# Kernel tuning notes

Hardware: AMD Instinct MI355X
Metric: run time of the kernel (lower is better)

Reference implementation:

```python
import jax, jax.numpy as jnp
import numpy as np

N_NODES = 100000
N_EDGES = 10000
N_PAIRS = 1600000
F = 128


def setup_inputs() -> dict:
    key = jax.random.key(0)
    ks = jax.random.split(key, 7)
    x = jax.random.normal(ks[0], (N_NODES, F), dtype=jnp.float32)
    action = jax.random.uniform(ks[1], (N_NODES, 3), dtype=jnp.float32)
    W_msg = jax.random.normal(ks[2], (F, F), dtype=jnp.float32) * (1.0 / np.sqrt(F))
    W_upd = jax.random.normal(ks[3], (F, F), dtype=jnp.float32) * (1.0 / np.sqrt(F))
    b_upd = jax.random.normal(ks[4], (F,), dtype=jnp.float32) * 0.02
    pair_node = jax.random.randint(ks[5], (N_PAIRS,), 0, N_NODES, dtype=jnp.int32)
    pair_edge = jax.random.randint(ks[6], (N_PAIRS,), 0, N_EDGES, dtype=jnp.int32)
    return {"x": x, "action": action, "W_msg": W_msg, "W_upd": W_upd,
            "b_upd": b_upd, "pair_node": pair_node, "pair_edge": pair_edge}


def _v2v_mean(m, pair_node, pair_edge):
    # v2e: mean of incident node features per hyperedge, then
    # e2v: mean of incident hyperedge features per node.
    ones = jnp.ones((pair_node.shape[0],), dtype=m.dtype)
    edge_deg = jax.ops.segment_sum(ones, pair_edge, num_segments=N_EDGES)
    node_deg = jax.ops.segment_sum(ones, pair_node, num_segments=N_NODES)
    # gather node features to incidence pairs, reduce into edges  [E, F]
    e_feat = jax.ops.segment_sum(m[pair_node], pair_edge, num_segments=N_EDGES)
    e_feat = e_feat / jnp.maximum(edge_deg, 1.0)[:, None]
    # gather edge features back to pairs, reduce into nodes       [N, F]
    v_feat = jax.ops.segment_sum(e_feat[pair_edge], pair_node, num_segments=N_NODES)
    v_feat = v_feat / jnp.maximum(node_deg, 1.0)[:, None]
    return v_feat


def reference(x, action, W_msg, W_upd, b_upd, pair_node, pair_edge):
    send = action[:, 0] + action[:, 2]      # [N]
    receive = action[:, 0] + action[:, 1]   # [N]
    m_ji = x @ W_msg.T                       # lin_message (no bias)
    m_ji = jax.nn.gelu(m_ji, approximate=False)  # dropout=0 (eval)
    m_ji = m_ji * send[:, None]
    m_i = _v2v_mean(m_ji, pair_node, pair_edge)
    m_i = m_i * receive[:, None]
    h_i = jax.nn.gelu(x @ W_upd.T + b_upd + m_i, approximate=False)
    return h_i
```

## Files before the change

### kernel.cpp

```cpp
#include <hip/hip_runtime.h>

#define N_NODESC 100000
#define N_EDGESC 10000
#define N_PAIRSC 1600000
#define FDIM 128

#define NB 200
#define EPB 50
#define NPB 500
#define ECAP2 8704
#define PA_CHUNK 8192
#define PA_NCH ((N_PAIRSC + PA_CHUNK - 1) / PA_CHUNK)
#define MSG_BLKS 782

typedef short bf16x8 __attribute__((ext_vector_type(8)));
typedef float f32x4 __attribute__((ext_vector_type(4)));
typedef float f32x2 __attribute__((ext_vector_type(2)));
typedef int i32x4 __attribute__((ext_vector_type(4)));
typedef unsigned u32x4 __attribute__((ext_vector_type(4)));

__device__ __forceinline__ unsigned short f2b(float f) {
  unsigned u = __float_as_uint(f);
  u += 0x7fffu + ((u >> 16) & 1u);
  return (unsigned short)(u >> 16);
}
__device__ __forceinline__ float b2f(unsigned short b) {
  return __uint_as_float(((unsigned)b) << 16);
}
__device__ __forceinline__ unsigned pack2(float a, float b) {
  return (unsigned)f2b(a) | ((unsigned)f2b(b) << 16);
}
__device__ __forceinline__ float gelu_fast(float z) {
  float z2 = z * z;
  float w = fmaf(0.044715f, z2, 1.0f);
  float e = __expf(1.5957691216f * z * w);
  return z * e * __builtin_amdgcn_rcpf(e + 1.0f);
}
__device__ __forceinline__ bf16x8 ldA(const float* p) {
  float4 u0 = *(const float4*)p;
  float4 u1 = *(const float4*)(p + 4);
  u32x4 w = {pack2(u0.x, u0.y), pack2(u0.z, u0.w), pack2(u1.x, u1.y), pack2(u1.z, u1.w)};
  return __builtin_bit_cast(bf16x8, w);
}

__global__ __launch_bounds__(256) void k_prep(const float* __restrict__ action,
                                              const float* __restrict__ wmsg, const float* __restrict__ wupd,
                                              short* __restrict__ wmsgb, short* __restrict__ wupdb,
                                              float* __restrict__ send, float* __restrict__ recv,
                                              int* __restrict__ gcure, int* __restrict__ gcurn) {
  int i = blockIdx.x * 256 + threadIdx.x;
  if (i < FDIM * FDIM) {
    wmsgb[i] = (short)f2b(wmsg[i]);
    wupdb[i] = (short)f2b(wupd[i]);
  }
  if (i < N_NODESC) {
    float a0 = action[i * 3 + 0], a1 = action[i * 3 + 1], a2 = action[i * 3 + 2];
    send[i] = a0 + a2;
    recv[i] = a0 + a1;
  }
  if (i < NB) {
    gcure[i] = i * ECAP2;
    gcurn[i] = i * ECAP2;
  }
}

__device__ __forceinline__ int wave_incl_scan(int v, int lane) {
#pragma unroll
  for (int d = 1; d < 64; d <<= 1) {
    int n = __shfl_up(v, d, 64);
    if (lane >= d) v += n;
  }
  return v;
}

__global__ __launch_bounds__(256) void k_part_msg(const int* __restrict__ pn, const int* __restrict__ pe,
                                                  int* __restrict__ gcure, int* __restrict__ gcurn,
                                                  unsigned* __restrict__ buckE, unsigned* __restrict__ buckN,
                                                  const float* __restrict__ x, const short* __restrict__ wb,
                                                  const float* __restrict__ send,
                                                  unsigned char* __restrict__ mji8) {
  __shared__ unsigned stage[PA_CHUNK];
  __shared__ int ce[NB], cn[NB];
  int t = threadIdx.x;
  if (blockIdx.x < PA_NCH) {
    for (int i = t; i < NB; i += 256) { ce[i] = 0; cn[i] = 0; }
    __syncthreads();
    long long base = (long long)blockIdx.x * PA_CHUNK;
    int nItems = (int)(((long long)N_PAIRSC - base) < PA_CHUNK ? (N_PAIRSC - base) : PA_CHUNK);
    for (int q = t; q < PA_CHUNK / 4; q += 256) {
      long long idx = base + (long long)q * 4;
      if (idx >= N_PAIRSC) break;
      i32x4 e4 = __builtin_nontemporal_load((const i32x4*)(pe + idx));
      i32x4 v4 = __builtin_nontemporal_load((const i32x4*)(pn + idx));
#pragma unroll
      for (int j = 0; j < 4; j++) {
        unsigned ee = (unsigned)e4[j], vv = (unsigned)v4[j];
        stage[q + j * (PA_CHUNK / 4)] = (ee << 17) | vv;
        atomicAdd(&ce[ee / EPB], 1);
        atomicAdd(&cn[vv / NPB], 1);
      }
    }
    __syncthreads();
    for (int i = t; i < NB; i += 256) {
      ce[i] = atomicAdd(&gcure[i], ce[i]);
      cn[i] = atomicAdd(&gcurn[i], cn[i]);
    }
    __syncthreads();
    for (int i = t; i < PA_CHUNK; i += 256) {
      int q = i & (PA_CHUNK / 4 - 1), j = i >> 11;
      long long idx = base + (long long)q * 4 + j;
      if (idx >= N_PAIRSC) continue;
      unsigned u = stage[i];
      unsigned ee = u >> 17, vv = u & 0x1FFFF;
      int p1 = atomicAdd(&ce[ee / EPB], 1);
      buckE[p1] = u;
      int p2 = atomicAdd(&cn[vv / NPB], 1);
      buckN[p2] = (vv << 14) | ee;
    }
    (void)nItems;
  } else {
    int gw = ((int)(blockIdx.x - PA_NCH) * 256 + t) >> 6;
    int lane = t & 63;
    if (gw >= N_NODESC / 32) return;
    int rb = gw * 32;
    int lr = lane & 15, lg = lane >> 4;

    bf16x8 A0[4], A1[4];
    const float* xrow0 = x + (size_t)(rb + lr) * FDIM + lg * 8;
    const float* xrow1 = xrow0 + 16 * FDIM;
#pragma unroll
    for (int kk = 0; kk < 4; kk++) {
      A0[kk] = ldA(xrow0 + kk * 32);
      A1[kk] = ldA(xrow1 + kk * 32);
    }
    float sv0[4], sv1[4];
#pragma unroll
    for (int j = 0; j < 4; j++) {
      sv0[j] = send[rb + lg * 4 + j];
      sv1[j] = send[rb + 16 + lg * 4 + j];
    }
#pragma unroll
    for (int c = 0; c < 8; c++) {
      f32x4 acc0 = {0.f, 0.f, 0.f, 0.f}, acc1 = {0.f, 0.f, 0.f, 0.f};
      const short* wrow = wb + (size_t)(16 * c + lr) * FDIM + lg * 8;
#pragma unroll
      for (int kk = 0; kk < 4; kk++) {
        bf16x8 B = *(const bf16x8*)(wrow + kk * 32);
        acc0 = __builtin_amdgcn_mfma_f32_16x16x32_bf16(A0[kk], B, acc0, 0, 0, 0);
        acc1 = __builtin_amdgcn_mfma_f32_16x16x32_bf16(A1[kk], B, acc1, 0, 0, 0);
      }
      int col = 16 * c + lr;
#pragma unroll
      for (int j = 0; j < 4; j++) {
        float m0 = gelu_fast(acc0[j]) * sv0[j];
        float m1 = gelu_fast(acc1[j]) * sv1[j];
        int row0 = rb + lg * 4 + j;
        mji8[(size_t)row0 * FDIM + col] =
            (unsigned char)(__builtin_amdgcn_cvt_pk_fp8_f32(m0, m0, 0, false) & 0xFF);
        mji8[(size_t)(row0 + 16) * FDIM + col] =
            (unsigned char)(__builtin_amdgcn_cvt_pk_fp8_f32(m1, m1, 0, false) & 0xFF);
      }
    }
  }
}

__global__ __launch_bounds__(256) void k_fine_e(const unsigned* __restrict__ buckE,
                                                const int* __restrict__ gcure,
                                                int* __restrict__ ecnt, int* __restrict__ eoff,
                                                int* __restrict__ sn) {
  __shared__ int cnt_s[EPB], cur_s[EPB];
  int b = blockIdx.x, t = threadIdx.x;
  int lo = b * EPB, beg = b * ECAP2, end = gcure[b];
  if (t < EPB) cnt_s[t] = 0;
  __syncthreads();
  for (int i = beg + t; i < end; i += 256)
    atomicAdd(&cnt_s[(int)(buckE[i] >> 17) - lo], 1);
  __syncthreads();
  if (t < 64) {
    int v = (t < EPB) ? cnt_s[t] : 0;
    int inc = wave_incl_scan(v, t);
    if (t < EPB) cur_s[t] = beg + inc - v;
  }
  __syncthreads();
  if (t < EPB) {
    ecnt[lo + t] = cnt_s[t];
    eoff[lo + t] = cur_s[t];
  }
  __syncthreads();
  for (int i = beg + t; i < end; i += 256) {
    unsigned u = buckE[i];
    int key = (int)(u >> 17) - lo;
    int pos = atomicAdd(&cur_s[key], 1);
    sn[pos] = (int)(u & 0x1FFFF);
  }
}

__global__ __launch_bounds__(256) void k_edge_fineN(const unsigned* __restrict__ buckN,
                                                    const int* __restrict__ gcurn,
                                                    int* __restrict__ ncnt, int* __restrict__ noff,
                                                    int* __restrict__ se,
                                                    const unsigned char* __restrict__ mji8,
                                                    const int* __restrict__ sn,
                                                    const int* __restrict__ eoff, const int* __restrict__ ecnt,
                                                    unsigned char* __restrict__ efeat8) {
  __shared__ int cnt_s[NPB], cur_s[NPB];
  int t = threadIdx.x;
  if (blockIdx.x < NB) {
    int b = blockIdx.x;
    int lo = b * NPB, beg = b * ECAP2, end = gcurn[b];
    for (int i = t; i < NPB; i += 256) cnt_s[i] = 0;
    __syncthreads();
    for (int i = beg + t; i < end; i += 256)
      atomicAdd(&cnt_s[(int)(buckN[i] >> 14) - lo], 1);
    __syncthreads();
    if (t < 64) {
      int carry = beg;
#pragma unroll
      for (int base = 0; base < NPB; base += 64) {
        int idx = base + t;
        int v = (idx < NPB) ? cnt_s[idx] : 0;
        int inc = wave_incl_scan(v, t);
        if (idx < NPB) cur_s[idx] = carry + inc - v;
        carry += __shfl(inc, 63, 64);
      }
    }
    __syncthreads();
    for (int i = t; i < NPB; i += 256) {
      ncnt[lo + i] = cnt_s[i];
      noff[lo + i] = cur_s[i];
    }
    __syncthreads();
    for (int i = beg + t; i < end; i += 256) {
      unsigned u = buckN[i];
      int key = (int)(u >> 14) - lo;
      int pos = atomicAdd(&cur_s[key], 1);
      se[pos] = (int)(u & 0x3FFF);
    }
  } else {
    int wave = (int)(blockIdx.x - NB) * 4 + (t >> 6);
    int lane = t & 63;
    int half = lane >> 5, sub2 = (lane >> 4) & 1, c4 = lane & 15;
    int edge = wave * 2 + half;
    if (edge >= N_EDGESC) return;
    int beg = eoff[edge], cnt = ecnt[edge];
    f32x2 a0 = {0.f, 0.f}, a1 = {0.f, 0.f}, a2 = {0.f, 0.f}, a3 = {0.f, 0.f};
#pragma unroll 4
    for (int p = sub2; p < cnt; p += 2) {
      int node = sn[beg + p];
      uint2 u = ((const uint2*)(mji8 + (size_t)node * FDIM))[c4];
      a0 += __builtin_amdgcn_cvt_pk_f32_fp8(u.x, false);
      a1 += __builtin_amdgcn_cvt_pk_f32_fp8(u.x, true);
      a2 += __builtin_amdgcn_cvt_pk_f32_fp8(u.y, false);
      a3 += __builtin_amdgcn_cvt_pk_f32_fp8(u.y, true);
    }
    a0[0] += __shfl_xor(a0[0], 16, 64); a0[1] += __shfl_xor(a0[1], 16, 64);
    a1[0] += __shfl_xor(a1[0], 16, 64); a1[1] += __shfl_xor(a1[1], 16, 64);
    a2[0] += __shfl_xor(a2[0], 16, 64); a2[1] += __shfl_xor(a2[1], 16, 64);
    a3[0] += __shfl_xor(a3[0], 16, 64); a3[1] += __shfl_xor(a3[1], 16, 64);
    if (sub2 == 0) {
      float inv = 1.0f / fmaxf((float)cnt, 1.0f);
      uint2 o;
      o.x = (unsigned)__builtin_amdgcn_cvt_pk_fp8_f32(a0[0] * inv, a0[1] * inv, 0, false);
      o.x = (unsigned)__builtin_amdgcn_cvt_pk_fp8_f32(a1[0] * inv, a1[1] * inv, (int)o.x, true);
      o.y = (unsigned)__builtin_amdgcn_cvt_pk_fp8_f32(a2[0] * inv, a2[1] * inv, 0, false);
      o.y = (unsigned)__builtin_amdgcn_cvt_pk_fp8_f32(a3[0] * inv, a3[1] * inv, (int)o.y, true);
      ((uint2*)(efeat8 + (size_t)edge * FDIM))[c4] = o;
    }
  }
}

__global__ __launch_bounds__(256) void k_node(const unsigned char* __restrict__ efeat8, const int* __restrict__ se,
                                              const int* __restrict__ noff, const int* __restrict__ ncnt,
                                              const float* __restrict__ recv, short* __restrict__ mi) {
  int wave = blockIdx.x * 4 + (threadIdx.x >> 6);
  int lane = threadIdx.x & 63;
  int sub = lane >> 4, c4 = lane & 15;
  int node = wave * 4 + sub;
  int beg = noff[node], cnt = ncnt[node];
  f32x2 a0 = {0.f, 0.f}, a1 = {0.f, 0.f}, a2 = {0.f, 0.f}, a3 = {0.f, 0.f};
#pragma unroll 4
  for (int p = 0; p < cnt; p++) {
    int e = se[beg + p];
    uint2 u = ((const uint2*)(efeat8 + (size_t)e * FDIM))[c4];
    a0 += __builtin_amdgcn_cvt_pk_f32_fp8(u.x, false);
    a1 += __builtin_amdgcn_cvt_pk_f32_fp8(u.x, true);
    a2 += __builtin_amdgcn_cvt_pk_f32_fp8(u.y, false);
    a3 += __builtin_amdgcn_cvt_pk_f32_fp8(u.y, true);
  }
  float s = recv[node] / fmaxf((float)cnt, 1.0f);
  u32x4 o;
  o[0] = pack2(a0[0] * s, a0[1] * s);
  o[1] = pack2(a1[0] * s, a1[1] * s);
  o[2] = pack2(a2[0] * s, a2[1] * s);
  o[3] = pack2(a3[0] * s, a3[1] * s);
  ((u32x4*)(mi + (size_t)node * FDIM))[c4] = o;
}

__global__ __launch_bounds__(256) void k_gemm_upd(const float* __restrict__ x, const short* __restrict__ wb,
                                                  const float* __restrict__ bias, const short* __restrict__ mi,
                                                  float* __restrict__ out) {
  int gw = (blockIdx.x * 256 + threadIdx.x) >> 6;
  int lane = threadIdx.x & 63;
  if (gw >= N_NODESC / 32) return;
  int rb = gw * 32;
  int lr = lane & 15, lg = lane >> 4;

  bf16x8 A0[4], A1[4];
  const float* xrow0 = x + (size_t)(rb + lr) * FDIM + lg * 8;
  const float* xrow1 = xrow0 + 16 * FDIM;
#pragma unroll
  for (int kk = 0; kk < 4; kk++) {
    A0[kk] = ldA(xrow0 + kk * 32);
    A1[kk] = ldA(xrow1 + kk * 32);
  }

#pragma unroll
  for (int c = 0; c < 8; c++) {
    f32x4 acc0 = {0.f, 0.f, 0.f, 0.f}, acc1 = {0.f, 0.f, 0.f, 0.f};
    const short* wrow = wb + (size_t)(16 * c + lr) * FDIM + lg * 8;
#pragma unroll
    for (int kk = 0; kk < 4; kk++) {
      bf16x8 B = *(const bf16x8*)(wrow + kk * 32);
      acc0 = __builtin_amdgcn_mfma_f32_16x16x32_bf16(A0[kk], B, acc0, 0, 0, 0);
      acc1 = __builtin_amdgcn_mfma_f32_16x16x32_bf16(A1[kk], B, acc1, 0, 0, 0);
    }
    int col = 16 * c + lr;
    float bc = bias[col];
#pragma unroll
    for (int j = 0; j < 4; j++) {
      int row0 = rb + lg * 4 + j;
      float z0 = acc0[j] + bc + b2f(((const unsigned short*)mi)[(size_t)row0 * FDIM + col]);
      float z1 = acc1[j] + bc + b2f(((const unsigned short*)mi)[(size_t)(row0 + 16) * FDIM + col]);
      __builtin_nontemporal_store(gelu_fast(z0), &out[(size_t)row0 * FDIM + col]);
      __builtin_nontemporal_store(gelu_fast(z1), &out[(size_t)(row0 + 16) * FDIM + col]);
    }
  }
}

extern "C" void kernel_launch(void* const* d_in, const int* in_sizes, int n_in,
                              void* d_out, int out_size, void* d_ws, size_t ws_size,
                              hipStream_t stream) {
  const float* x = (const float*)d_in[0];
  const float* action = (const float*)d_in[1];
  const float* wmsg = (const float*)d_in[2];
  const float* wupd = (const float*)d_in[3];
  const float* bupd = (const float*)d_in[4];
  const int* pn = (const int*)d_in[5];
  const int* pe = (const int*)d_in[6];
  float* out = (float*)d_out;

  char* p = (char*)d_ws;
  auto alloc = [&](size_t bytes) -> char* {
    char* r = p;
    p += (bytes + 255) & ~(size_t)255;
    return r;
  };
  unsigned char* mji8 = (unsigned char*)alloc((size_t)N_NODESC * FDIM);
  short* mi = (short*)alloc((size_t)N_NODESC * FDIM * 2);
  unsigned char* efeat8 = (unsigned char*)alloc((size_t)N_EDGESC * FDIM);
  int* sn = (int*)alloc((size_t)NB * ECAP2 * 4);
  int* se = (int*)alloc((size_t)NB * ECAP2 * 4);
  short* wmsgb = (short*)alloc(FDIM * FDIM * 2);
  short* wupdb = (short*)alloc(FDIM * FDIM * 2);
  float* send = (float*)alloc(N_NODESC * 4);
  float* recv = (float*)alloc(N_NODESC * 4);
  int* ecnt = (int*)alloc(N_EDGESC * 4);
  int* eoff = (int*)alloc(N_EDGESC * 4);
  int* ncnt = (int*)alloc(N_NODESC * 4);
  int* noff = (int*)alloc(N_NODESC * 4);
  int* gcure = (int*)alloc(NB * 4);
  int* gcurn = (int*)alloc(NB * 4);

  unsigned* buckE = (unsigned*)mi;
  unsigned* buckN = buckE + (size_t)NB * ECAP2;

  k_prep<<<391, 256, 0, stream>>>(action, wmsg, wupd, wmsgb, wupdb, send, recv, gcure, gcurn);
  k_part_msg<<<PA_NCH + MSG_BLKS, 256, 0, stream>>>(pn, pe, gcure, gcurn, buckE, buckN,
                                                    x, wmsgb, send, mji8);
  k_fine_e<<<NB, 256, 0, stream>>>(buckE, gcure, ecnt, eoff, sn);
  k_edge_fineN<<<NB + 1250, 256, 0, stream>>>(buckN, gcurn, ncnt, noff, se,
                                              mji8, sn, eoff, ecnt, efeat8);
  k_node<<<6250, 256, 0, stream>>>(efeat8, se, noff, ncnt, recv, mi);
  k_gemm_upd<<<782, 256, 0, stream>>>(x, wupdb, bupd, mi, out);
}
```

Measured before the change: 164.4 us.

## Store node messages as fp8, shrink partition chunks, use per-wave LDS bucket counters

```diff
diff --git a/kernel.cpp b/kernel.cpp
--- a/kernel.cpp
+++ b/kernel.cpp
@@ -9,7 +9,7 @@
 #define EPB 50
 #define NPB 500
 #define ECAP2 8704
-#define PA_CHUNK 8192
+#define PA_CHUNK 4096
 #define PA_NCH ((N_PAIRSC + PA_CHUNK - 1) / PA_CHUNK)
 #define MSG_BLKS 782
 
@@ -80,13 +80,13 @@
                                                   const float* __restrict__ send,
                                                   unsigned char* __restrict__ mji8) {
   __shared__ unsigned stage[PA_CHUNK];
-  __shared__ int ce[NB], cn[NB];
+  __shared__ int ce4[4][NB], cn4[4][NB];
   int t = threadIdx.x;
   if (blockIdx.x < PA_NCH) {
-    for (int i = t; i < NB; i += 256) { ce[i] = 0; cn[i] = 0; }
+    int w = t >> 6;
+    for (int i = t; i < 4 * NB; i += 256) { ((int*)ce4)[i] = 0; ((int*)cn4)[i] = 0; }
     __syncthreads();
     long long base = (long long)blockIdx.x * PA_CHUNK;
-    int nItems = (int)(((long long)N_PAIRSC - base) < PA_CHUNK ? (N_PAIRSC - base) : PA_CHUNK);
     for (int q = t; q < PA_CHUNK / 4; q += 256) {
       long long idx = base + (long long)q * 4;
       if (idx >= N_PAIRSC) break;
@@ -96,28 +96,31 @@
       for (int j = 0; j < 4; j++) {
         unsigned ee = (unsigned)e4[j], vv = (unsigned)v4[j];
         stage[q + j * (PA_CHUNK / 4)] = (ee << 17) | vv;
-        atomicAdd(&ce[ee / EPB], 1);
-        atomicAdd(&cn[vv / NPB], 1);
+        atomicAdd(&ce4[w][ee / EPB], 1);
+        atomicAdd(&cn4[w][vv / NPB], 1);
       }
     }
     __syncthreads();
-    for (int i = t; i < NB; i += 256) {
-      ce[i] = atomicAdd(&gcure[i], ce[i]);
-      cn[i] = atomicAdd(&gcurn[i], cn[i]);
+    if (t < NB) {
+      int c0 = ce4[0][t], c1 = ce4[1][t], c2 = ce4[2][t], c3 = ce4[3][t];
+      int b0 = atomicAdd(&gcure[t], c0 + c1 + c2 + c3);
+      ce4[0][t] = b0; ce4[1][t] = b0 + c0; ce4[2][t] = b0 + c0 + c1; ce4[3][t] = b0 + c0 + c1 + c2;
+      int d0 = cn4[0][t], d1 = cn4[1][t], d2 = cn4[2][t], d3 = cn4[3][t];
+      int b1 = atomicAdd(&gcurn[t], d0 + d1 + d2 + d3);
+      cn4[0][t] = b1; cn4[1][t] = b1 + d0; cn4[2][t] = b1 + d0 + d1; cn4[3][t] = b1 + d0 + d1 + d2;
     }
     __syncthreads();
     for (int i = t; i < PA_CHUNK; i += 256) {
-      int q = i & (PA_CHUNK / 4 - 1), j = i >> 11;
+      int q = i & (PA_CHUNK / 4 - 1), j = i >> 10;
       long long idx = base + (long long)q * 4 + j;
       if (idx >= N_PAIRSC) continue;
       unsigned u = stage[i];
       unsigned ee = u >> 17, vv = u & 0x1FFFF;
-      int p1 = atomicAdd(&ce[ee / EPB], 1);
+      int p1 = atomicAdd(&ce4[w][ee / EPB], 1);
       buckE[p1] = u;
-      int p2 = atomicAdd(&cn[vv / NPB], 1);
+      int p2 = atomicAdd(&cn4[w][vv / NPB], 1);
       buckN[p2] = (vv << 14) | ee;
     }
-    (void)nItems;
   } else {
     int gw = ((int)(blockIdx.x - PA_NCH) * 256 + t) >> 6;
     int lane = t & 63;
@@ -271,7 +274,7 @@
 
 __global__ __launch_bounds__(256) void k_node(const unsigned char* __restrict__ efeat8, const int* __restrict__ se,
                                               const int* __restrict__ noff, const int* __restrict__ ncnt,
-                                              const float* __restrict__ recv, short* __restrict__ mi) {
+                                              const float* __restrict__ recv, unsigned char* __restrict__ mi8) {
   int wave = blockIdx.x * 4 + (threadIdx.x >> 6);
   int lane = threadIdx.x & 63;
   int sub = lane >> 4, c4 = lane & 15;
@@ -288,16 +291,17 @@
     a3 += __builtin_amdgcn_cvt_pk_f32_fp8(u.y, true);
   }
   float s = recv[node] / fmaxf((float)cnt, 1.0f);
-  u32x4 o;
-  o[0] = pack2(a0[0] * s, a0[1] * s);
-  o[1] = pack2(a1[0] * s, a1[1] * s);
-  o[2] = pack2(a2[0] * s, a2[1] * s);
-  o[3] = pack2(a3[0] * s, a3[1] * s);
-  ((u32x4*)(mi + (size_t)node * FDIM))[c4] = o;
+  uint2 o;
+  o.x = (unsigned)__builtin_amdgcn_cvt_pk_fp8_f32(a0[0] * s, a0[1] * s, 0, false);
+  o.x = (unsigned)__builtin_amdgcn_cvt_pk_fp8_f32(a1[0] * s, a1[1] * s, (int)o.x, true);
+  o.y = (unsigned)__builtin_amdgcn_cvt_pk_fp8_f32(a2[0] * s, a2[1] * s, 0, false);
+  o.y = (unsigned)__builtin_amdgcn_cvt_pk_fp8_f32(a3[0] * s, a3[1] * s, (int)o.y, true);
+  ((uint2*)(mi8 + (size_t)node * FDIM))[c4] = o;
 }
 
 __global__ __launch_bounds__(256) void k_gemm_upd(const float* __restrict__ x, const short* __restrict__ wb,
-                                                  const float* __restrict__ bias, const short* __restrict__ mi,
+                                                  const float* __restrict__ bias,
+                                                  const unsigned char* __restrict__ mi8,
                                                   float* __restrict__ out) {
   int gw = (blockIdx.x * 256 + threadIdx.x) >> 6;
   int lane = threadIdx.x & 63;
@@ -329,8 +333,10 @@
 #pragma unroll
     for (int j = 0; j < 4; j++) {
       int row0 = rb + lg * 4 + j;
-      float z0 = acc0[j] + bc + b2f(((const unsigned short*)mi)[(size_t)row0 * FDIM + col]);
-      float z1 = acc1[j] + bc + b2f(((const unsigned short*)mi)[(size_t)(row0 + 16) * FDIM + col]);
+      f32x2 m0 = __builtin_amdgcn_cvt_pk_f32_fp8((unsigned)mi8[(size_t)row0 * FDIM + col], false);
+      f32x2 m1 = __builtin_amdgcn_cvt_pk_f32_fp8((unsigned)mi8[(size_t)(row0 + 16) * FDIM + col], false);
+      float z0 = acc0[j] + bc + m0[0];
+      float z1 = acc1[j] + bc + m1[0];
       __builtin_nontemporal_store(gelu_fast(z0), &out[(size_t)row0 * FDIM + col]);
       __builtin_nontemporal_store(gelu_fast(z1), &out[(size_t)(row0 + 16) * FDIM + col]);
     }
@@ -356,8 +362,10 @@
     return r;
   };
   unsigned char* mji8 = (unsigned char*)alloc((size_t)N_NODESC * FDIM);
-  short* mi = (short*)alloc((size_t)N_NODESC * FDIM * 2);
+  unsigned char* mi8 = (unsigned char*)alloc((size_t)N_NODESC * FDIM);
   unsigned char* efeat8 = (unsigned char*)alloc((size_t)N_EDGESC * FDIM);
+  unsigned* buckE = (unsigned*)alloc((size_t)NB * ECAP2 * 4);
+  unsigned* buckN = (unsigned*)alloc((size_t)NB * ECAP2 * 4);
   int* sn = (int*)alloc((size_t)NB * ECAP2 * 4);
   int* se = (int*)alloc((size_t)NB * ECAP2 * 4);
   short* wmsgb = (short*)alloc(FDIM * FDIM * 2);
@@ -371,15 +379,12 @@
   int* gcure = (int*)alloc(NB * 4);
   int* gcurn = (int*)alloc(NB * 4);
 
-  unsigned* buckE = (unsigned*)mi;
-  unsigned* buckN = buckE + (size_t)NB * ECAP2;
-
   k_prep<<<391, 256, 0, stream>>>(action, wmsg, wupd, wmsgb, wupdb, send, recv, gcure, gcurn);
   k_part_msg<<<PA_NCH + MSG_BLKS, 256, 0, stream>>>(pn, pe, gcure, gcurn, buckE, buckN,
                                                     x, wmsgb, send, mji8);
   k_fine_e<<<NB, 256, 0, stream>>>(buckE, gcure, ecnt, eoff, sn);
   k_edge_fineN<<<NB + 1250, 256, 0, stream>>>(buckN, gcurn, ncnt, noff, se,
                                               mji8, sn, eoff, ecnt, efeat8);
-  k_node<<<6250, 256, 0, stream>>>(efeat8, se, noff, ncnt, recv, mi);
-  k_gemm_upd<<<782, 256, 0, stream>>>(x, wupdb, bupd, mi, out);
-}
+  k_node<<<6250, 256, 0, stream>>>(efeat8, se, noff, ncnt, recv, mi8);
+  k_gemm_upd<<<782, 256, 0, stream>>>(x, wupdb, bupd, mi8, out);
+}
```

Measured after the change: 171.2 us. 1.04x slower.
